# Kernel optimization log

Measured on AMD Instinct MI355X. Metric: run time of the kernel, lower is better.

## Reference

```python
import jax, jax.numpy as jnp
import numpy as np

B, S, D, H = 2, 2048, 2048, 16
HD = D // H            # 128
HALF = HD // 2         # 64
SOFTCAP = 50.0
ROPE_BASE = 10000.0


def setup_inputs() -> dict:
    key = jax.random.key(0)
    k1, k2, k3 = jax.random.split(key, 3)
    inputs = jax.random.normal(k1, (B, S, D), dtype=jnp.float32)
    # param init ~ nnx.initializers.normal() (stddev 0.01 default; scale to keep activations sane)
    w_in = jax.random.normal(k2, (D, H, 3 * HD), dtype=jnp.float32) * (1.0 / np.sqrt(D))
    w_out = jax.random.normal(k3, (H, HD, D), dtype=jnp.float32) * (1.0 / np.sqrt(D))
    # RoPE tables: [S, HALF]
    pos = jnp.arange(S, dtype=jnp.float32)[:, None]
    inv_freq = 1.0 / (ROPE_BASE ** (jnp.arange(HALF, dtype=jnp.float32) / HALF))
    ang = pos * inv_freq[None, :]
    rope_sin = jnp.sin(ang)
    rope_cos = jnp.cos(ang)
    # causal mask [1, 1, S, S]
    mask = jnp.tril(jnp.ones((S, S), dtype=bool))[None, None, :, :]
    return {"inputs": inputs, "w_in": w_in, "w_out": w_out,
            "rope_sin": rope_sin, "rope_cos": rope_cos, "mask": mask}


def apply_rope(x, sin, cos):
    # x: [B, S, H, HD]; sin/cos: [S, HALF] -> broadcast [1, S, 1, HALF]
    sin = sin[None, :, None, :]
    cos = cos[None, :, None, :]
    x1, x2 = x[..., :HALF], x[..., HALF:]
    return jnp.concatenate([x1 * cos - x2 * sin, x2 * cos + x1 * sin], axis=-1)


def reference(inputs, w_in, w_out, rope_sin, rope_cos, mask):
    dtype = inputs.dtype
    # fused QKV projection: [B, S, H, 3*HD]
    qkv = jnp.einsum('bsd,bhf->bshf'.replace('bhf', 'dhf'), inputs, w_in)
    q, k, v = jnp.split(qkv, 3, axis=-1)           # each [B, S, H, HD]
    q = apply_rope(q, rope_sin, rope_cos)
    k = apply_rope(k, rope_sin, rope_cos)
    q = q / jnp.sqrt(jnp.asarray(HD, dtype))
    scores = jnp.einsum('bqhd,bkhd->bhqk', q, k)   # [B, H, S, S]
    big_neg = jnp.finfo(dtype).min
    scores = jnp.where(mask, scores, big_neg)
    scores = jnp.tanh(scores / SOFTCAP) * SOFTCAP  # softcap
    attn = jax.nn.softmax(scores, axis=-1)
    x = jnp.einsum('bhqk,bkhd->bqhd', attn, v)     # [B, S, H, HD]
    out = jnp.einsum('bqhd,hdm->bqm', x, w_out)    # [B, S, D]
    return out
```

## Files before the change

### kernel.cpp

```cpp
#include <hip/hip_runtime.h>

#define B_ 2
#define S_ 2048
#define D_ 2048
#define H_ 16
#define HD_ 128
#define NT_ (S_ / 64)

typedef unsigned short u16;
typedef __bf16 bf16x8 __attribute__((ext_vector_type(8)));
typedef float f32x4 __attribute__((ext_vector_type(4)));
typedef u16 u16x8 __attribute__((ext_vector_type(8)));

__device__ __forceinline__ float bf2f(u16 u) {
  unsigned int x = ((unsigned int)u) << 16;
  return __builtin_bit_cast(float, x);
}
__device__ __forceinline__ u16 f2bf(float f) {
  unsigned int u = __builtin_bit_cast(unsigned int, f);
  u += 0x7fffu + ((u >> 16) & 1u);
  return (u16)(u >> 16);
}
__device__ __forceinline__ void async16(const void* g, void* l) {
  __builtin_amdgcn_global_load_lds((const __attribute__((address_space(1))) void*)g,
                                   (__attribute__((address_space(3))) void*)l, 16, 0, 0);
}
__device__ __forceinline__ float vexp2(float x) {
  float r;
  asm("v_exp_f32 %0, %1" : "=v"(r) : "v"(x));
  return r;
}
__device__ __forceinline__ float vrcp(float x) {
  float r;
  asm("v_rcp_f32 %0, %1" : "=v"(r) : "v"(x));
  return r;
}

__global__ __launch_bounds__(256) void conv_f32_bf16(const float* __restrict__ in,
                                                     u16* __restrict__ outp, int n) {
  int idx = (blockIdx.x * 256 + threadIdx.x) * 4;
  int stride = gridDim.x * 256 * 4;
  for (; idx < n; idx += stride) {
    float4 v = *(const float4*)(in + idx);
    ushort4 ov = make_ushort4(f2bf(v.x), f2bf(v.y), f2bf(v.z), f2bf(v.w));
    *(ushort4*)(outp + idx) = ov;
  }
}

__global__ __launch_bounds__(256) void transpose_win(const float* __restrict__ in,
                                                     u16* __restrict__ outp) {
  __shared__ float tile[32][33];
  int n0 = blockIdx.x * 32, k0 = blockIdx.y * 32;
  int tx = threadIdx.x & 31, ty = threadIdx.x >> 5;
  int n = n0 + tx;
  int cc = n >> 7, p = n & 127;
  int q = (p >> 4) & 3;
  int d = ((p >> 6) << 5) + ((q >> 1) << 4) + ((q & 1) << 6) + (p & 15);
  int f = (cc / 3) * 384 + (cc % 3) * 128 + d;
#pragma unroll
  for (int yy = 0; yy < 32; yy += 8)
    tile[ty + yy][tx] = in[(size_t)(k0 + ty + yy) * 6144 + f];
  __syncthreads();
#pragma unroll
  for (int yy = 0; yy < 32; yy += 8)
    outp[(size_t)(n0 + ty + yy) * 2048 + k0 + tx] = f2bf(tile[tx][ty + yy]);
}

__global__ __launch_bounds__(256) void transpose_wout(const float* __restrict__ in,
                                                      u16* __restrict__ outp) {
  __shared__ float tile[32][33];
  int k0 = blockIdx.x * 32, n0 = blockIdx.y * 32;
  int tx = threadIdx.x & 31, ty = threadIdx.x >> 5;
#pragma unroll
  for (int yy = 0; yy < 32; yy += 8) {
    int kk = k0 + ty + yy;
    int hh = kk >> 7, j = kk & 127;
    int hd = (j & 7) * 16 + (j >> 3);
    tile[ty + yy][tx] = in[(size_t)(hh * 128 + hd) * 2048 + n0 + tx];
  }
  __syncthreads();
#pragma unroll
  for (int yy = 0; yy < 32; yy += 8)
    outp[(size_t)(n0 + ty + yy) * 2048 + k0 + tx] = f2bf(tile[tx][ty + yy]);
}

#define BAR __builtin_amdgcn_s_barrier()
#define LGKM0                                          \
  {                                                    \
    asm volatile("s_waitcnt lgkmcnt(0)" ::: "memory"); \
    __builtin_amdgcn_sched_barrier(0);                 \
  }
#define VM6 asm volatile("s_waitcnt vmcnt(6)" ::: "memory")
#define VM0 asm volatile("s_waitcnt vmcnt(0)" ::: "memory")
#define P1 __builtin_amdgcn_s_setprio(1)
#define P0 __builtin_amdgcn_s_setprio(0)

template <int EPI>
__global__ __launch_bounds__(512, 1) void gemm128(
    const u16* __restrict__ A, const u16* __restrict__ Bt, float* __restrict__ C, int K, int N,
    int ntn, u16* __restrict__ Qo, u16* __restrict__ Ko, u16* __restrict__ Vo,
    const float* __restrict__ rsin, const float* __restrict__ rcos) {
  __shared__ alignas(16) u16 lsA[3][128 * 64];
  __shared__ alignas(16) u16 lsB[3][256 * 64];
  const int tid = threadIdx.x;
  const int lane = tid & 63, wid = tid >> 6;
  const int g = lane >> 4, lr = lane & 15;
  const int wm = wid >> 2, wn = wid & 3;

  const int nwg = ntn << 5;
  const int bid = blockIdx.x;
  const int swz = (bid & 7) * (nwg >> 3) + (bid >> 3);
  const int m_idx = swz & 31, n_idx = swz >> 5;
  const size_t m0 = (size_t)m_idx * 128, n0 = (size_t)n_idx * 256;

  const int rowq = tid >> 3, slq = tid & 7;
  const int kofs = (slq ^ (rowq & 7)) << 3;
  const u16* pA0 = A + (m0 + rowq) * K + kofs;
  const u16* pA1 = A + (m0 + 64 + rowq) * K + kofs;
  const u16* pB0 = Bt + (n0 + rowq) * K + kofs;
  const u16* pB1 = Bt + (n0 + 64 + rowq) * K + kofs;
  const u16* pB2 = Bt + (n0 + 128 + rowq) * K + kofs;
  const u16* pB3 = Bt + (n0 + 192 + rowq) * K + kofs;

#define STG_A(t, buf)                                                 \
  {                                                                   \
    async16(pA0 + (size_t)(t)*64, (char*)lsA[buf] + tid * 16);        \
    async16(pA1 + (size_t)(t)*64, (char*)lsA[buf] + 8192 + tid * 16); \
  }
#define STG_B(t, buf)                                                  \
  {                                                                    \
    async16(pB0 + (size_t)(t)*64, (char*)lsB[buf] + tid * 16);         \
    async16(pB1 + (size_t)(t)*64, (char*)lsB[buf] + 8192 + tid * 16);  \
    async16(pB2 + (size_t)(t)*64, (char*)lsB[buf] + 16384 + tid * 16); \
    async16(pB3 + (size_t)(t)*64, (char*)lsB[buf] + 24576 + tid * 16); \
  }

  const int sw0 = ((g) ^ (lr & 7)) << 4;
  const int sw1 = ((4 + g) ^ (lr & 7)) << 4;

#define LDA(tb)                                                               \
  {                                                                           \
    _Pragma("unroll") for (int i2 = 0; i2 < 4; ++i2) {                        \
      const char* _p = (const char*)lsA[tb] + (wm * 64 + i2 * 16 + lr) * 128; \
      aF[i2][0] = *(const bf16x8*)(_p + sw0);                                 \
      aF[i2][1] = *(const bf16x8*)(_p + sw1);                                 \
    }                                                                         \
  }
#define LDB(tb, dst, nh)                                                                \
  {                                                                                     \
    _Pragma("unroll") for (int j2 = 0; j2 < 2; ++j2) {                                  \
      const char* _p = (const char*)lsB[tb] + (wn * 64 + (nh)*32 + j2 * 16 + lr) * 128; \
      dst[j2][0] = *(const bf16x8*)(_p + sw0);                                          \
      dst[j2][1] = *(const bf16x8*)(_p + sw1);                                          \
    }                                                                                   \
  }
#define MM(nh, BB)                                                                           \
  {                                                                                          \
    _Pragma("unroll") for (int i2 = 0; i2 < 4; ++i2) _Pragma("unroll") for (int j2 = 0;     \
                                                                            j2 < 2; ++j2) { \
      acc[i2][(nh)*2 + j2] = __builtin_amdgcn_mfma_f32_16x16x32_bf16(                        \
          aF[i2][0], BB[j2][0], acc[i2][(nh)*2 + j2], 0, 0, 0);                              \
      acc[i2][(nh)*2 + j2] = __builtin_amdgcn_mfma_f32_16x16x32_bf16(                        \
          aF[i2][1], BB[j2][1], acc[i2][(nh)*2 + j2], 0, 0, 0);                              \
    }                                                                                        \
  }

  f32x4 acc[4][4] = {};
  const int nk = K >> 6;

  STG_A(0, 0);
  STG_B(0, 0);
  STG_A(1, 1);
  STG_B(1, 1);
  VM6;
  BAR;

  bf16x8 aF[4][2], b01[2][2], b23[2][2];
#pragma unroll 1
  for (int kt = 0; kt < nk; ++kt) {
    const int tb = kt % 3;
    const int sb = (kt + 2) % 3;
    const bool stg = (kt + 2) < nk;
    LDA(tb);
    LDB(tb, b01, 0);
    if (stg) STG_A(kt + 2, sb);
    BAR;
    LGKM0;
    P1;
    MM(0, b01);
    P0;
    BAR;
    LDB(tb, b23, 1);
    if (stg) STG_B(kt + 2, sb);
    BAR;
    LGKM0;
    P1;
    MM(1, b23);
    P0;
    if (kt < nk - 2) {
      VM6;
    } else {
      VM0;
    }
    BAR;
  }
#undef STG_A
#undef STG_B
#undef LDA
#undef LDB
#undef MM

  if (EPI == 0) {
#pragma unroll
    for (int i = 0; i < 4; ++i)
#pragma unroll
      for (int j = 0; j < 4; ++j)
#pragma unroll
        for (int r = 0; r < 4; ++r) {
          size_t m = m0 + wm * 64 + i * 16 + 4 * g + r;
          size_t n = n0 + wn * 64 + j * 16 + lr;
          C[m * N + n] = acc[i][j][r];
        }
  } else {
    const int c = (int)(n0 >> 7) + (wn >> 1);
    const int h = c / 3, part = c % 3;
    const int wn1 = wn & 1;
    if (part == 2) {
#pragma unroll
      for (int i = 0; i < 4; ++i) {
        int m = (int)m0 + wm * 64 + i * 16 + 4 * g;
        int b = m >> 11, s = m & (S_ - 1);
#pragma unroll
        for (int j = 0; j < 4; ++j) {
          int hd = wn1 * 32 + ((j >> 1) << 4) + ((j & 1) << 6) + lr;
          ushort4 pk;
          pk.x = f2bf(acc[i][j][0]);
          pk.y = f2bf(acc[i][j][1]);
          pk.z = f2bf(acc[i][j][2]);
          pk.w = f2bf(acc[i][j][3]);
          *(ushort4*)(Vo + ((size_t)(b * H_ + h) * HD_ + hd) * S_ + s) = pk;
        }
      }
    } else {
      u16* dstp = (part == 0) ? Qo : Ko;
      const float scl = (part == 0) ? 0.08838834764831845f : 1.0f;
#pragma unroll
      for (int i = 0; i < 4; ++i) {
        int mbase = (int)m0 + wm * 64 + i * 16 + 4 * g;
#pragma unroll
        for (int r = 0; r < 4; ++r) {
          int m = mbase + r;
          int b = m >> 11, s = m & (S_ - 1);
          const float* srow = rsin + s * 64;
          const float* crow = rcos + s * 64;
          u16* op = dstp + ((size_t)(b * H_ + h) * S_ + s) * HD_ + ((wn1 * 16 + lr) << 2);
          ushort4 pk;
          {
            int d = wn1 * 32 + lr;
            float cv = crow[d] * scl, sv = srow[d] * scl;
            float x1 = acc[i][0][r], x2 = acc[i][1][r];
            pk.x = f2bf(x1 * cv - x2 * sv);
            pk.y = f2bf(x2 * cv + x1 * sv);
          }
          {
            int d = wn1 * 32 + 16 + lr;
            float cv = crow[d] * scl, sv = srow[d] * scl;
            float x1 = acc[i][2][r], x2 = acc[i][3][r];
            pk.z = f2bf(x1 * cv - x2 * sv);
            pk.w = f2bf(x2 * cv + x1 * sv);
          }
          *(ushort4*)op = pk;
        }
      }
    }
  }
}

__global__ __launch_bounds__(256) void attn_fwd(const u16* __restrict__ Q, const u16* __restrict__ K,
                                                const u16* __restrict__ VT, u16* __restrict__ X) {
  const int bx = blockIdx.x;
  const int bh = blockIdx.y;
  const int tid = threadIdx.x;
  const int lane = tid & 63, wid = tid >> 6;
  const int g = lane >> 4, lr = lane & 15;

  __shared__ alignas(16) u16 lsK[2][64 * 128];
  __shared__ alignas(16) u16 lsV[2][128 * 64];
  __shared__ alignas(16) u16 lsP[4][16 * 72];

  const u16* Qp = Q + (size_t)bh * S_ * HD_;
  const u16* Kp = K + (size_t)bh * S_ * HD_;
  const u16* Vp = VT + (size_t)bh * HD_ * S_;
  u16* myP = lsP[wid];
  const int b = bh >> 4, h = bh & 15;

  const float c1 = -0.057707802f;
  const float c2 = -144.26950409f;

#pragma unroll 1
  for (int pass = 0; pass < 2; ++pass) {
    const int qt = pass ? bx : (NT_ - 1 - bx);
    const int qq = qt * 64 + wid * 16 + lr;

    bf16x8 qf[4];
#pragma unroll
    for (int kc = 0; kc < 4; ++kc)
      qf[kc] = *(const bf16x8*)(Qp + (size_t)qq * HD_ + kc * 32 + g * 8);

    f32x4 o[8] = {};
    float psum = 0.f;

#pragma unroll
    for (int p = 0; p < 4; ++p) {
      int c = p * 256 + tid;
      int rowk = c >> 4;
      int wsk = ((c & 15) << 4) ^ ((rowk & 7) << 4);
      async16((const char*)Kp + (((size_t)rowk) << 8) + wsk, (char*)lsK[0] + c * 16);
      int rowv = c >> 3;
      int wsv = ((c & 7) << 4) ^ ((rowv & 7) << 4);
      async16((const char*)Vp + (size_t)rowv * (S_ * 2) + wsv, (char*)lsV[0] + c * 16);
    }
    __syncthreads();

    int cur = 0;
    for (int kt = 0; kt <= qt; ++kt) {
      if (kt < qt) {
        const int nxt = kt + 1;
#pragma unroll
        for (int p = 0; p < 4; ++p) {
          int c = p * 256 + tid;
          int rowk = c >> 4;
          int wsk = ((c & 15) << 4) ^ ((rowk & 7) << 4);
          async16((const char*)Kp + (((size_t)(nxt * 64 + rowk)) << 8) + wsk,
                  (char*)lsK[cur ^ 1] + c * 16);
          int rowv = c >> 3;
          int wsv = ((c & 7) << 4) ^ ((rowv & 7) << 4);
          async16((const char*)Vp + (size_t)rowv * (S_ * 2) + nxt * 128 + wsv,
                  (char*)lsV[cur ^ 1] + c * 16);
        }
      }
      f32x4 sc[4];
#pragma unroll
      for (int jn = 0; jn < 4; ++jn) {
        f32x4 a = {0.f, 0.f, 0.f, 0.f};
        const int row = jn * 16 + lr;
        const int sw = (row & 7) << 4;
#pragma unroll
        for (int kc = 0; kc < 4; ++kc) {
          int w = (kc * 64 + g * 16) ^ sw;
          bf16x8 kf = *(const bf16x8*)((const char*)lsK[cur] + row * 256 + w);
          a = __builtin_amdgcn_mfma_f32_16x16x32_bf16(kf, qf[kc], a, 0, 0, 0);
        }
        sc[jn] = a;
      }
#pragma unroll
      for (int jn = 0; jn < 4; ++jn) {
        const int kbase = kt * 64 + jn * 16 + 4 * g;
        float pv[4];
#pragma unroll
        for (int r = 0; r < 4; ++r) {
          float z = vexp2(c1 * sc[jn][r]);
          float p = vexp2(c2 * z * vrcp(1.f + z));
          if (kbase + r > qq) p = 0.f;
          psum += p;
          pv[r] = p;
        }
        unsigned int w0 = (unsigned int)f2bf(pv[0]) | ((unsigned int)f2bf(pv[1]) << 16);
        unsigned int w1 = (unsigned int)f2bf(pv[2]) | ((unsigned int)f2bf(pv[3]) << 16);
        *(uint2*)(myP + lr * 72 + jn * 16 + 4 * g) = make_uint2(w0, w1);
      }
#pragma unroll
      for (int kc = 0; kc < 2; ++kc) {
        bf16x8 pa = *(const bf16x8*)(myP + lr * 72 + kc * 32 + g * 8);
#pragma unroll
        for (int jh = 0; jh < 8; ++jh) {
          int row = jh * 16 + lr;
          int w = (kc * 64 + g * 16) ^ ((row & 7) << 4);
          bf16x8 vf = *(const bf16x8*)((const char*)lsV[cur] + row * 128 + w);
          o[jh] = __builtin_amdgcn_mfma_f32_16x16x32_bf16(pa, vf, o[jh], 0, 0, 0);
        }
      }
      __syncthreads();
      cur ^= 1;
    }
    float s = psum;
    s += __shfl_xor(s, 16, 64);
    s += __shfl_xor(s, 32, 64);
    const int qbo = qt * 64 + wid * 16 + 4 * g;
#pragma unroll
    for (int r = 0; r < 4; ++r) {
      float ls = __shfl(s, (lane & 48) | (4 * g + r), 64);
      float inv = 1.f / ls;
      int sq = qbo + r;
      u16x8 pk;
#pragma unroll
      for (int jh = 0; jh < 8; ++jh) pk[jh] = f2bf(o[jh][r] * inv);
      *(u16x8*)(X + ((size_t)(b * S_ + sq)) * D_ + h * HD_ + lr * 8) = pk;
    }
  }
}

extern "C" void kernel_launch(void* const* d_in, const int* in_sizes, int n_in,
                              void* d_out, int out_size, void* d_ws, size_t ws_size,
                              hipStream_t stream) {
  const float* inputs = (const float*)d_in[0];
  const float* w_in = (const float*)d_in[1];
  const float* w_out = (const float*)d_in[2];
  const float* rsin = (const float*)d_in[3];
  const float* rcos = (const float*)d_in[4];
  float* out = (float*)d_out;

  char* ws = (char*)d_ws;
  u16* bfA = (u16*)(ws);
  u16* w_inT = (u16*)(ws + 16777216);
  u16* Qraw = (u16*)(ws + 41943040);
  u16* Kraw = (u16*)(ws + 58720256);
  u16* VT = (u16*)(ws + 75497472);
  u16* Xbuf = (u16*)(ws);
  u16* w_outT = (u16*)(ws + 16777216);

  conv_f32_bf16<<<2048, 256, 0, stream>>>(inputs, bfA, B_ * S_ * D_);
  transpose_win<<<dim3(192, 64), 256, 0, stream>>>(w_in, w_inT);
  gemm128<1><<<768, 512, 0, stream>>>(bfA, w_inT, nullptr, 2048, 6144, 24, Qraw, Kraw, VT,
                                      rsin, rcos);
  transpose_wout<<<dim3(64, 64), 256, 0, stream>>>(w_out, w_outT);
  attn_fwd<<<dim3(NT_ / 2, 32), 256, 0, stream>>>(Qraw, Kraw, VT, Xbuf);
  gemm128<0><<<256, 512, 0, stream>>>(Xbuf, w_outT, out, 2048, 2048, 8,
                                      nullptr, nullptr, nullptr, nullptr, nullptr);
}
```

Measured before the change: 279.1 us.

## Shrink GEMM K-tile to 32 with single-phase MFMA loop and new LDS swizzle

Halves the K-tile from 64 to 32. LDS use per stage drops, and each iteration now does one load phase followed by 16 MFMAs instead of two split half-phases. The staging layout, swizzle and waitcnt depth are reworked to match: three async loads per stage, with the wait at vmcnt(3). This removes one barrier pair per 32-K slice, but the loop runs twice as many iterations, so barrier and wait overhead per unit of K roughly doubles and each stage hides less latency.

Result: no change. 276.6 us (-0.9%).

```diff
diff --git a/kernel.cpp b/kernel.cpp
--- a/kernel.cpp
+++ b/kernel.cpp
@@ -90,7 +90,7 @@
     asm volatile("s_waitcnt lgkmcnt(0)" ::: "memory"); \
     __builtin_amdgcn_sched_barrier(0);                 \
   }
-#define VM6 asm volatile("s_waitcnt vmcnt(6)" ::: "memory")
+#define VM3 asm volatile("s_waitcnt vmcnt(3)" ::: "memory")
 #define VM0 asm volatile("s_waitcnt vmcnt(0)" ::: "memory")
 #define P1 __builtin_amdgcn_s_setprio(1)
 #define P0 __builtin_amdgcn_s_setprio(0)
@@ -100,8 +100,8 @@
     const u16* __restrict__ A, const u16* __restrict__ Bt, float* __restrict__ C, int K, int N,
     int ntn, u16* __restrict__ Qo, u16* __restrict__ Ko, u16* __restrict__ Vo,
     const float* __restrict__ rsin, const float* __restrict__ rcos) {
-  __shared__ alignas(16) u16 lsA[3][128 * 64];
-  __shared__ alignas(16) u16 lsB[3][256 * 64];
+  __shared__ alignas(16) u16 lsA[3][128 * 32];
+  __shared__ alignas(16) u16 lsB[3][256 * 32];
   const int tid = threadIdx.x;
   const int lane = tid & 63, wid = tid >> 6;
   const int g = lane >> 4, lr = lane & 15;
@@ -113,102 +113,65 @@
   const int m_idx = swz & 31, n_idx = swz >> 5;
   const size_t m0 = (size_t)m_idx * 128, n0 = (size_t)n_idx * 256;
 
-  const int rowq = tid >> 3, slq = tid & 7;
-  const int kofs = (slq ^ (rowq & 7)) << 3;
-  const u16* pA0 = A + (m0 + rowq) * K + kofs;
-  const u16* pA1 = A + (m0 + 64 + rowq) * K + kofs;
-  const u16* pB0 = Bt + (n0 + rowq) * K + kofs;
-  const u16* pB1 = Bt + (n0 + 64 + rowq) * K + kofs;
-  const u16* pB2 = Bt + (n0 + 128 + rowq) * K + kofs;
-  const u16* pB3 = Bt + (n0 + 192 + rowq) * K + kofs;
-
-#define STG_A(t, buf)                                                 \
-  {                                                                   \
-    async16(pA0 + (size_t)(t)*64, (char*)lsA[buf] + tid * 16);        \
-    async16(pA1 + (size_t)(t)*64, (char*)lsA[buf] + 8192 + tid * 16); \
-  }
-#define STG_B(t, buf)                                                  \
-  {                                                                    \
-    async16(pB0 + (size_t)(t)*64, (char*)lsB[buf] + tid * 16);         \
-    async16(pB1 + (size_t)(t)*64, (char*)lsB[buf] + 8192 + tid * 16);  \
-    async16(pB2 + (size_t)(t)*64, (char*)lsB[buf] + 16384 + tid * 16); \
-    async16(pB3 + (size_t)(t)*64, (char*)lsB[buf] + 24576 + tid * 16); \
-  }
-
-  const int sw0 = ((g) ^ (lr & 7)) << 4;
-  const int sw1 = ((4 + g) ^ (lr & 7)) << 4;
-
-#define LDA(tb)                                                               \
-  {                                                                           \
-    _Pragma("unroll") for (int i2 = 0; i2 < 4; ++i2) {                        \
-      const char* _p = (const char*)lsA[tb] + (wm * 64 + i2 * 16 + lr) * 128; \
-      aF[i2][0] = *(const bf16x8*)(_p + sw0);                                 \
-      aF[i2][1] = *(const bf16x8*)(_p + sw1);                                 \
-    }                                                                         \
-  }
-#define LDB(tb, dst, nh)                                                                \
-  {                                                                                     \
-    _Pragma("unroll") for (int j2 = 0; j2 < 2; ++j2) {                                  \
-      const char* _p = (const char*)lsB[tb] + (wn * 64 + (nh)*32 + j2 * 16 + lr) * 128; \
-      dst[j2][0] = *(const bf16x8*)(_p + sw0);                                          \
-      dst[j2][1] = *(const bf16x8*)(_p + sw1);                                          \
-    }                                                                                   \
-  }
-#define MM(nh, BB)                                                                           \
-  {                                                                                          \
-    _Pragma("unroll") for (int i2 = 0; i2 < 4; ++i2) _Pragma("unroll") for (int j2 = 0;     \
-                                                                            j2 < 2; ++j2) { \
-      acc[i2][(nh)*2 + j2] = __builtin_amdgcn_mfma_f32_16x16x32_bf16(                        \
-          aF[i2][0], BB[j2][0], acc[i2][(nh)*2 + j2], 0, 0, 0);                              \
-      acc[i2][(nh)*2 + j2] = __builtin_amdgcn_mfma_f32_16x16x32_bf16(                        \
-          aF[i2][1], BB[j2][1], acc[i2][(nh)*2 + j2], 0, 0, 0);                              \
-    }                                                                                        \
+  const int rowA = tid >> 2, slA = tid & 3;
+  const int rowB0 = tid >> 2;
+  const int rowB1 = (512 + tid) >> 2;
+  const u16* srcA = A + (m0 + rowA) * K + ((slA ^ ((rowA >> 1) & 3)) << 3);
+  const u16* srcB0 = Bt + (n0 + rowB0) * K + ((slA ^ ((rowB0 >> 1) & 3)) << 3);
+  const u16* srcB1 = Bt + (n0 + rowB1) * K + ((slA ^ ((rowB1 >> 1) & 3)) << 3);
+
+#define STAGE(t, buf)                                                   \
+  {                                                                     \
+    const int koff = (t) << 5;                                          \
+    async16(srcA + koff, (char*)lsA[buf] + tid * 16);                   \
+    async16(srcB0 + koff, (char*)lsB[buf] + tid * 16);                  \
+    async16(srcB1 + koff, (char*)lsB[buf] + 8192 + tid * 16);           \
+  }
+
+  int ofsA[4], ofsB[4];
+#pragma unroll
+  for (int i = 0; i < 4; ++i) {
+    int ra = wm * 64 + i * 16 + lr;
+    ofsA[i] = ra * 64 + ((g ^ ((ra >> 1) & 3)) << 4);
+    int rb = wn * 64 + i * 16 + lr;
+    ofsB[i] = rb * 64 + ((g ^ ((rb >> 1) & 3)) << 4);
   }
 
   f32x4 acc[4][4] = {};
-  const int nk = K >> 6;
-
-  STG_A(0, 0);
-  STG_B(0, 0);
-  STG_A(1, 1);
-  STG_B(1, 1);
-  VM6;
+  const int nk = K >> 5;
+
+  STAGE(0, 0);
+  STAGE(1, 1);
+  VM3;
   BAR;
 
-  bf16x8 aF[4][2], b01[2][2], b23[2][2];
 #pragma unroll 1
   for (int kt = 0; kt < nk; ++kt) {
     const int tb = kt % 3;
     const int sb = (kt + 2) % 3;
-    const bool stg = (kt + 2) < nk;
-    LDA(tb);
-    LDB(tb, b01, 0);
-    if (stg) STG_A(kt + 2, sb);
+    bf16x8 aF[4], bF[4];
+#pragma unroll
+    for (int i = 0; i < 4; ++i) aF[i] = *(const bf16x8*)((const char*)lsA[tb] + ofsA[i]);
+#pragma unroll
+    for (int j = 0; j < 4; ++j) bF[j] = *(const bf16x8*)((const char*)lsB[tb] + ofsB[j]);
+    if (kt + 2 < nk) STAGE(kt + 2, sb);
     BAR;
     LGKM0;
     P1;
-    MM(0, b01);
-    P0;
-    BAR;
-    LDB(tb, b23, 1);
-    if (stg) STG_B(kt + 2, sb);
-    BAR;
-    LGKM0;
-    P1;
-    MM(1, b23);
+#pragma unroll
+    for (int i = 0; i < 4; ++i)
+#pragma unroll
+      for (int j = 0; j < 4; ++j)
+        acc[i][j] = __builtin_amdgcn_mfma_f32_16x16x32_bf16(aF[i], bF[j], acc[i][j], 0, 0, 0);
     P0;
     if (kt < nk - 2) {
-      VM6;
+      VM3;
     } else {
       VM0;
     }
     BAR;
   }
-#undef STG_A
-#undef STG_B
-#undef LDA
-#undef LDB
-#undef MM
+#undef STAGE
 
   if (EPI == 0) {
 #pragma unroll
```
